# Kernel optimization log

Measured on AMD Instinct MI355X. Metric: run time of the kernel, lower is better.

Reference implementation:

```python
import jax, jax.numpy as jnp
import numpy as np

E = 384      # EMBEDDING_SIZE
DFF = 1536
H = 6        # NUM_HEADS
D = E // H   # ATTN_DIM_SIZE = 64
T = 256      # SEQ_LEN
L = 6        # NUM_BLOCKS
V = 65       # VOCAB_SIZE
NPOS = 10000.0
B = 128


def _pos_encoding():
    i = jnp.arange(T, dtype=jnp.float32)[:, None]
    k = jnp.arange(E // 2, dtype=jnp.float32)[None, :]
    ang = i / jnp.power(NPOS, 2.0 * k / E)   # [T, E/2]
    pe = jnp.zeros((T, E), dtype=jnp.float32)
    pe = pe.at[:, 0::2].set(jnp.sin(ang))
    pe = pe.at[:, 1::2].set(jnp.cos(ang))
    return pe


def setup_inputs() -> dict:
    key = jax.random.key(0)
    ks = jax.random.split(key, 24)
    s = 0.02
    n = lambda k, shp: (jax.random.normal(k, shp, dtype=jnp.float32) * s)
    inp = {
        'tokens': jax.random.randint(ks[0], (B, T), 0, V),
        'pos_enc': _pos_encoding(),
        'emb': n(ks[1], (V, E)),
        # stacked per-layer params [L, ...]; weights stored as (in, out)
        'Wq': n(ks[2], (L, E, E)), 'bq': jnp.zeros((L, E)),
        'Wk': n(ks[3], (L, E, E)), 'bk': jnp.zeros((L, E)),
        'Wv': n(ks[4], (L, E, E)), 'bv': jnp.zeros((L, E)),
        'Wo': n(ks[5], (L, E, E)), 'bo': jnp.zeros((L, E)),
        'ln1_g': jnp.ones((L, E)), 'ln1_b': jnp.zeros((L, E)),
        'W1': n(ks[6], (L, E, DFF)), 'c1': jnp.zeros((L, DFF)),
        'W2': n(ks[7], (L, DFF, E)), 'c2': jnp.zeros((L, E)),
        'ln2_g': jnp.ones((L, E)), 'ln2_b': jnp.zeros((L, E)),
        'Wl': n(ks[8], (E, V)), 'bl': jnp.zeros((V,)),
    }
    return inp


def _layer_norm(x, g, b, eps=1e-5):
    mu = jnp.mean(x, axis=-1, keepdims=True)
    var = jnp.mean((x - mu) ** 2, axis=-1, keepdims=True)
    return (x - mu) * jax.lax.rsqrt(var + eps) * g + b


def _decoder(tokens, pos_enc, emb, Wq, bq, Wk, bk, Wv, bv, Wo, bo,
             ln1_g, ln1_b, W1, c1, W2, c2, ln2_g, ln2_b, Wl, bl):
    b_, t_ = tokens.shape
    x = emb[tokens] + pos_enc[None, :t_, :]            # [B,T,E]
    causal = jnp.tril(jnp.ones((t_, t_), dtype=bool)) # tril mask
    scale = D ** (-0.5)

    def block(x, p):
        (wq, bq_, wk, bk_, wv, bv_, wo, bo_, g1, be1, w1, c1_, w2, c2_, g2, be2) = p
        h = _layer_norm(x, g1, be1)
        q = (h @ wq + bq_).reshape(b_, t_, H, D)
        k = (h @ wk + bk_).reshape(b_, t_, H, D)
        v = (h @ wv + bv_).reshape(b_, t_, H, D)
        scores = jnp.einsum('bqhd,bkhd->bhqk', q, k) * scale
        scores = jnp.where(causal[None, None], scores, -jnp.inf)
        attn = jax.nn.softmax(scores, axis=-1)
        o = jnp.einsum('bhqk,bkhd->bqhd', attn, v).reshape(b_, t_, E)
        x = x + (o @ wo + bo_)
        h2 = _layer_norm(x, g2, be2)
        x = x + (jax.nn.relu(h2 @ w1 + c1_) @ w2 + c2_)
        return x, None

    params = (Wq, bq, Wk, bk, Wv, bv, Wo, bo, ln1_g, ln1_b, W1, c1, W2, c2, ln2_g, ln2_b)
    x, _ = jax.lax.scan(block, x, params)
    return x @ Wl + bl                                 # [B,T,V]


def reference(tokens, pos_enc, emb, Wq, bq, Wk, bk, Wv, bv, Wo, bo,
              ln1_g, ln1_b, W1, c1, W2, c2, ln2_g, ln2_b, Wl, bl):
    return _decoder(tokens, pos_enc, emb, Wq, bq, Wk, bk, Wv, bv, Wo, bo,
                    ln1_g, ln1_b, W1, c1, W2, c2, ln2_g, ln2_b, Wl, bl)
```

## Files before the change

kernel.cpp:

```cpp
#include <hip/hip_runtime.h>
#include <hip/hip_bf16.h>
#include <stdint.h>

constexpr int E   = 384;
constexpr int DFF = 1536;
constexpr int NH  = 6;
constexpr int HD  = 64;
constexpr int T   = 256;
constexpr int NL  = 6;
constexpr int NV  = 65;
constexpr int BB  = 128;
constexpr int MTOT = BB * T;
constexpr int CB  = 32;

typedef __bf16 bf16;
typedef __attribute__((ext_vector_type(8))) __bf16 bf16x8;
typedef __attribute__((ext_vector_type(4))) __bf16 bf16x4;
typedef __attribute__((ext_vector_type(4))) float floatx4;

__device__ __forceinline__ void gload_lds16(const void* g, void* l) {
    __builtin_amdgcn_global_load_lds(
        (const __attribute__((address_space(1))) void*)g,
        (__attribute__((address_space(3))) void*)l, 16, 0, 0);
}

#define GBN 128

template <int MODE, int SWAP, int W>
__device__ __forceinline__ void gemm_body(
    char* AsB,
    const bf16* __restrict__ A, int lda,
    const bf16* __restrict__ Bf,
    const float* __restrict__ bias,
    void* __restrict__ Cv, void* __restrict__ Cv2, int ldc,
    int nt, int mt, int Nvalid, int K, int relu)
{
    constexpr int BM     = W * 32;
    constexpr int ABYTES = BM * 64;
    constexpr int SBUF   = ABYTES + 8192;

    int tid = threadIdx.x;
    int lane = tid & 63;
    int wid = tid >> 6;
    int wr = wid >> 1, wc = wid & 1;
    int lq = lane >> 4, lr = lane & 15;

    const bf16* Ab = A + (long)mt * BM * lda;

    int rp0 = wid * 8 + (lane >> 3);
    int s   = lane & 7;
    int sp  = s ^ (rp0 & 7);
    int rowA = 2 * rp0 + (sp >> 2);
    int kOff = (sp & 3) * 8;
    const bf16* srcA0 = Ab + (long)rowA * lda + kOff;
    const bf16* srcA1 = srcA0 + (long)(BM / 2) * lda;
    int dst0 = wid * 1024;
    int dst1 = W * 1024 + wid * 1024;

    int nks = K / 32;

    const bf16* srcB0;
    const bf16* srcB1 = nullptr;
    int dstB0, dstB1 = 0;
    if constexpr (W == 8) {
        srcB0 = Bf + ((long)(nt * 8 + wid) * nks) * 512 + lane * 8;
        dstB0 = ABYTES + wid * 1024;
    } else {
        srcB0 = Bf + ((long)(nt * 8 + wid * 2) * nks) * 512 + lane * 8;
        srcB1 = Bf + ((long)(nt * 8 + wid * 2 + 1) * nks) * 512 + lane * 8;
        dstB0 = ABYTES + (wid * 2) * 1024;
        dstB1 = ABYTES + (wid * 2 + 1) * 1024;
    }

    floatx4 acc[4][4];
#pragma unroll
    for (int i = 0; i < 4; i++)
#pragma unroll
        for (int j = 0; j < 4; j++) acc[i][j] = floatx4{0.f, 0.f, 0.f, 0.f};

    int afo = (wr * 32 + (lr >> 1)) * 128 +
              (((((lr & 1) << 2) | lq) ^ (lr >> 1)) << 4);
    int bfo = ABYTES + wc * 4096 + lane * 16;

    auto stage = [&](int ks, int bo) {
        long ka = (long)ks * 32;
        gload_lds16(srcA0 + ka, AsB + bo + dst0);
        gload_lds16(srcA1 + ka, AsB + bo + dst1);
        long kb = (long)ks * 512;
        gload_lds16(srcB0 + kb, AsB + bo + dstB0);
        if constexpr (W == 4)
            gload_lds16(srcB1 + kb, AsB + bo + dstB1);
    };

    int o0 = 0, o1 = SBUF, o2 = 2 * SBUF;

    stage(0, o0);
    if (nks > 1) {
        stage(1, o1);
        if constexpr (W == 8)
            asm volatile("s_waitcnt vmcnt(3)" ::: "memory");
        else
            asm volatile("s_waitcnt vmcnt(4)" ::: "memory");
    } else {
        asm volatile("s_waitcnt vmcnt(0)" ::: "memory");
    }
    __builtin_amdgcn_s_barrier();

    for (int ki = 0; ki < nks; ++ki) {
        if (ki + 2 < nks) stage(ki + 2, o2);
        __builtin_amdgcn_sched_barrier(0);

        bf16x8 bfr[4];
#pragma unroll
        for (int ni = 0; ni < 4; ni++)
            bfr[ni] = *(const bf16x8*)(AsB + o0 + bfo + ni * 1024);
        bf16x8 af[4];
#pragma unroll
        for (int mi = 0; mi < 4; mi++)
            af[mi] = *(const bf16x8*)(AsB + o0 + afo + mi * 1024);

        __builtin_amdgcn_s_setprio(1);
#pragma unroll
        for (int mi = 0; mi < 4; mi++)
#pragma unroll
            for (int ni = 0; ni < 4; ni++)
                acc[mi][ni] = SWAP
                    ? __builtin_amdgcn_mfma_f32_16x16x32_bf16(bfr[ni], af[mi], acc[mi][ni], 0, 0, 0)
                    : __builtin_amdgcn_mfma_f32_16x16x32_bf16(af[mi], bfr[ni], acc[mi][ni], 0, 0, 0);
        __builtin_amdgcn_s_setprio(0);

        if (ki + 1 < nks) {
            if (ki + 2 < nks) {
                if constexpr (W == 8)
                    asm volatile("s_waitcnt vmcnt(3) lgkmcnt(0)" ::: "memory");
                else
                    asm volatile("s_waitcnt vmcnt(4) lgkmcnt(0)" ::: "memory");
            } else {
                asm volatile("s_waitcnt vmcnt(0) lgkmcnt(0)" ::: "memory");
            }
            __builtin_amdgcn_s_barrier();
        }
        int t = o0; o0 = o1; o1 = o2; o2 = t;
    }

    int m0 = mt * BM, n0 = nt * GBN;
#pragma unroll
    for (int mi = 0; mi < 4; mi++) {
#pragma unroll
        for (int ni = 0; ni < 4; ni++) {
            floatx4 v = acc[mi][ni];
            if (SWAP) {
                int rowL = m0 + wr * 64 + mi * 16 + lr;
                int col0 = n0 + wc * 64 + ni * 16 + lq * 4;
                if (MODE == 5) {
                    bf16x4 pv;
#pragma unroll
                    for (int r = 0; r < 4; r++) pv[r] = (bf16)(v[r] + bias[col0 + r]);
                    *(bf16x4*)((bf16*)Cv + (long)rowL * 768 + col0) = pv;
                } else if (MODE == 1) {
                    bf16* Cp = (bf16*)Cv;
                    bf16x4* ptr = (bf16x4*)(Cp + (long)rowL * ldc + col0);
                    bf16x4 old = *ptr;
                    bf16x4 pv;
#pragma unroll
                    for (int r = 0; r < 4; r++)
                        pv[r] = (bf16)((float)old[r] + v[r] + bias[col0 + r]);
                    *ptr = pv;
                } else if (MODE == 4) {
                    float* Cp = (float*)Cv;
#pragma unroll
                    for (int r = 0; r < 4; r++)
                        if (col0 + r < Nvalid)
                            Cp[(long)rowL * ldc + col0 + r] = v[r] + bias[col0 + r];
                } else {
                    if (col0 < Nvalid) {
                        bf16x4 pv;
#pragma unroll
                        for (int r = 0; r < 4; r++) {
                            float x = v[r] + (bias ? bias[col0 + r] : 0.f);
                            if (relu) x = fmaxf(x, 0.f);
                            pv[r] = (bf16)x;
                        }
                        *(bf16x4*)((bf16*)Cv + (long)rowL * ldc + col0) = pv;
                    }
                }
            } else {
                int row0 = m0 + wr * 64 + mi * 16 + lq * 4;
                int colL = n0 + wc * 64 + ni * 16 + lr;
                float bv = bias[colL];
                bf16x4 pv;
#pragma unroll
                for (int r = 0; r < 4; r++) pv[r] = (bf16)(v[r] + bv);
                int bidx = row0 >> 8, pos = row0 & 255, e = colL - 768;
                *(bf16x4*)((bf16*)Cv2 + (long)bidx * (E * T) + (long)e * T + pos) = pv;
            }
        }
    }
}

template <int MODE, int W>
__global__ __launch_bounds__(W * 64, 4) void k_gemm(
    const bf16* __restrict__ A, int lda,
    const bf16* __restrict__ Bf,
    const float* __restrict__ bias,
    void* __restrict__ Cv, void* __restrict__ Cv2, int ldc,
    int Mtiles, int Ntiles, int Nvalid, int K,
    int relu)
{
    __shared__ __align__(16) char AsB[3 * (W * 32 * 64 + 8192)];

    int nb = gridDim.x;
    int per = nb >> 3;
    int bphys = blockIdx.x;
    int bid = (bphys & 7) * per + (bphys >> 3);

    int nt = bid % Ntiles;
    int mt = bid / Ntiles;

    if (MODE == 5 && nt >= 6)
        gemm_body<5, 0, W>(AsB, A, lda, Bf, bias, Cv, Cv2, ldc, nt, mt, Nvalid, K, relu);
    else
        gemm_body<MODE, 1, W>(AsB, A, lda, Bf, bias, Cv, Cv2, ldc, nt, mt, Nvalid, K, relu);
}

__global__ __launch_bounds__(256) void k_attn(
    const bf16* __restrict__ qk, const bf16* __restrict__ vt,
    bf16* __restrict__ o)
{
    int nb = gridDim.x;
    int per = nb >> 3;
    int bphys = blockIdx.x;
    int bid = (bphys & 7) * per + (bphys >> 3);

    int qt = bid & 3; bid >>= 2;
    int h = bid % NH; int b = bid / NH;
    int tid = threadIdx.x;
    int lane = tid & 63;
    int w = tid >> 6;
    int lq = lane >> 4;
    int lr = lane & 15;

    __shared__ __align__(16) bf16 Ks[256 * 72];
    __shared__ __align__(16) bf16 Vs[64 * 264];

    const bf16* qbase = qk + (long)(b * T + qt * 64 + w * 16) * 768 + h * 64;
    const bf16* kbase = qk + (long)(b * T) * 768 + 384 + h * 64;
    const bf16* vbase = vt + ((long)b * E + h * 64) * T;

#pragma unroll
    for (int i = 0; i < 8; i++) {
        int idx = i * 256 + tid;
        int row = idx >> 3, off = (idx & 7) * 8;
        *(bf16x8*)(&Ks[row * 72 + off]) = *(const bf16x8*)(kbase + (long)row * 768 + off);
    }
#pragma unroll
    for (int i = 0; i < 8; i++) {
        int idx = i * 256 + tid;
        int row = idx >> 5, off = (idx & 31) * 8;
        *(bf16x8*)(&Vs[row * 264 + off]) = *(const bf16x8*)(vbase + (long)row * 256 + off);
    }

    bf16x8 aq0 = *(const bf16x8*)(qbase + (long)lr * 768 + lq * 8);
    bf16x8 aq1 = *(const bf16x8*)(qbase + (long)lr * 768 + 32 + lq * 8);

    __syncthreads();

    const int ntmax = qt * 4 + 3;
    floatx4 zero = {0.f, 0.f, 0.f, 0.f};
    floatx4 s[16];
#pragma unroll
    for (int nt = 0; nt < 16; nt++) s[nt] = zero;

#pragma unroll
    for (int nt = 0; nt < 16; nt++) {
        if (nt <= ntmax) {
            const bf16* kp = &Ks[(nt * 16 + lr) * 72 + lq * 8];
            bf16x8 b0 = *(const bf16x8*)(kp);
            bf16x8 b1 = *(const bf16x8*)(kp + 32);
            s[nt] = __builtin_amdgcn_mfma_f32_16x16x32_bf16(aq0, b0, s[nt], 0, 0, 0);
            s[nt] = __builtin_amdgcn_mfma_f32_16x16x32_bf16(aq1, b1, s[nt], 0, 0, 0);
        }
    }

    int trow0 = qt * 64 + w * 16 + lq * 4;
    float m4[4] = {-3e38f, -3e38f, -3e38f, -3e38f};
#pragma unroll
    for (int nt = 0; nt < 16; nt++) {
        if (nt <= ntmax) {
            int tc = nt * 16 + lr;
#pragma unroll
            for (int r = 0; r < 4; r++) {
                float v = s[nt][r] * 0.125f;
                if (tc > trow0 + r) v = -3e38f;
                s[nt][r] = v;
                m4[r] = fmaxf(m4[r], v);
            }
        }
    }
#pragma unroll
    for (int r = 0; r < 4; r++) {
#pragma unroll
        for (int off = 1; off < 16; off <<= 1)
            m4[r] = fmaxf(m4[r], __shfl_xor(m4[r], off, 64));
    }

    float l4[4] = {0.f, 0.f, 0.f, 0.f};
#pragma unroll
    for (int nt = 0; nt < 16; nt++) {
        if (nt <= ntmax) {
#pragma unroll
            for (int r = 0; r < 4; r++) {
                float pv = __expf(s[nt][r] - m4[r]);
                l4[r] += pv;
                s[nt][r] = pv;
            }
        }
    }
#pragma unroll
    for (int r = 0; r < 4; r++) {
#pragma unroll
        for (int off = 1; off < 16; off <<= 1)
            l4[r] += __shfl_xor(l4[r], off, 64);
    }

    __syncthreads();

    bf16* P = Ks + w * (16 * 264);
#pragma unroll
    for (int nt = 0; nt < 16; nt++) {
        if (nt <= ntmax) {
#pragma unroll
            for (int r = 0; r < 4; r++)
                P[(lq * 4 + r) * 264 + nt * 16 + lr] = (bf16)s[nt][r];
        }
    }

    floatx4 oacc[4];
#pragma unroll
    for (int nd = 0; nd < 4; nd++) oacc[nd] = zero;
    const int kkmax = 2 * (qt + 1);
#pragma unroll
    for (int kk = 0; kk < 8; kk++) {
        if (kk < kkmax) {
            bf16x8 ap = *(const bf16x8*)(&P[lr * 264 + kk * 32 + lq * 8]);
#pragma unroll
            for (int nd = 0; nd < 4; nd++) {
                bf16x8 bv = *(const bf16x8*)(&Vs[(nd * 16 + lr) * 264 + kk * 32 + lq * 8]);
                oacc[nd] = __builtin_amdgcn_mfma_f32_16x16x32_bf16(ap, bv, oacc[nd], 0, 0, 0);
            }
        }
    }

#pragma unroll
    for (int r = 0; r < 4; r++) {
        float inv = 1.0f / l4[r];
        long rowg = (long)b * T + trow0 + r;
#pragma unroll
        for (int nd = 0; nd < 4; nd++) {
            o[rowg * E + h * 64 + nd * 16 + lr] = (bf16)(oacc[nd][r] * inv);
        }
    }
}

__global__ void k_ln(const bf16* __restrict__ x, const float* __restrict__ g,
                     const float* __restrict__ b, bf16* __restrict__ h) {
    int row = blockIdx.x * 4 + (threadIdx.x >> 6);
    int lane = threadIdx.x & 63;
    const bf16* xr = x + (long)row * E;
    float v[6];
    float s = 0.f;
#pragma unroll
    for (int i = 0; i < 6; i++) { v[i] = (float)xr[lane + 64 * i]; s += v[i]; }
#pragma unroll
    for (int o = 1; o < 64; o <<= 1) s += __shfl_xor(s, o, 64);
    float mu = s * (1.0f / E);
    float q = 0.f;
#pragma unroll
    for (int i = 0; i < 6; i++) { float d = v[i] - mu; q += d * d; }
#pragma unroll
    for (int o = 1; o < 64; o <<= 1) q += __shfl_xor(q, o, 64);
    float rs = rsqrtf(q * (1.0f / E) + 1e-5f);
    bf16* hr = h + (long)row * E;
#pragma unroll
    for (int i = 0; i < 6; i++) {
        int c = lane + 64 * i;
        hr[c] = (bf16)((v[i] - mu) * rs * g[c] + b[c]);
    }
}

__global__ void k_transpose_frag(const float* __restrict__ W, bf16* __restrict__ Wf,
                                 int K, int N, int NPAD) {
    long idx = (long)blockIdx.x * 256 + threadIdx.x;
    long per = (long)NPAD * K;
    int l = (int)(idx / per);
    long r = idx - (long)l * per;
    int j = (int)(r & 7); r >>= 3;
    int lane = (int)(r & 63); r >>= 6;
    int nks = K / 32;
    int ks = (int)(r % nks);
    int c16 = (int)(r / nks);
    int col = c16 * 16 + (lane & 15);
    int k = ks * 32 + (lane >> 4) * 8 + j;
    Wf[idx] = (col < N) ? (bf16)W[((long)l * K + k) * N + col] : (bf16)0.0f;
}

__global__ void k_transpose_qkv_frag(const float* __restrict__ Wq, const float* __restrict__ Wk,
                                     const float* __restrict__ Wv, bf16* __restrict__ Wf) {
    long idx = (long)blockIdx.x * 256 + threadIdx.x;
    long per = (long)1152 * E;
    int l = (int)(idx / per);
    long r = idx - (long)l * per;
    int j = (int)(r & 7); r >>= 3;
    int lane = (int)(r & 63); r >>= 6;
    int nks = E / 32;
    int ks = (int)(r % nks);
    int c16 = (int)(r / nks);
    int col = c16 * 16 + (lane & 15);
    int k = ks * 32 + (lane >> 4) * 8 + j;
    const float* src;
    int cc;
    if (col < 384)      { src = Wq; cc = col; }
    else if (col < 768) { src = Wk; cc = col - 384; }
    else                { src = Wv; cc = col - 768; }
    Wf[idx] = (bf16)src[((long)l * E + k) * E + cc];
}

__global__ void k_bias_qkv(const float* __restrict__ bq, const float* __restrict__ bk,
                           const float* __restrict__ bv, float* __restrict__ bqkv) {
    int idx = blockIdx.x * 256 + threadIdx.x;
    int l = idx / 1152;
    int j = idx - l * 1152;
    const float* src;
    int jj;
    if (j < 384)      { src = bq; jj = j; }
    else if (j < 768) { src = bk; jj = j - 384; }
    else              { src = bv; jj = j - 768; }
    bqkv[idx] = src[l * E + jj];
}

__global__ void k_embed(const int* __restrict__ tokens, const float* __restrict__ pos,
                        const float* __restrict__ emb, bf16* __restrict__ x) {
    long idx = (long)blockIdx.x * 256 + threadIdx.x;
    int e = (int)(idx % E);
    long bt = idx / E;
    int t = (int)(bt % T);
    int tok = tokens[bt];
    x[idx] = (bf16)(emb[(long)tok * E + e] + pos[(long)t * E + e]);
}

extern "C" void kernel_launch(void* const* d_in, const int* in_sizes, int n_in,
                              void* d_out, int out_size, void* d_ws, size_t ws_size,
                              hipStream_t stream) {
    const int*   tokens = (const int*)d_in[0];
    const float* pos  = (const float*)d_in[1];
    const float* emb  = (const float*)d_in[2];
    const float* Wq   = (const float*)d_in[3];
    const float* bq   = (const float*)d_in[4];
    const float* Wk   = (const float*)d_in[5];
    const float* bk   = (const float*)d_in[6];
    const float* Wv   = (const float*)d_in[7];
    const float* bv   = (const float*)d_in[8];
    const float* Wo   = (const float*)d_in[9];
    const float* bo   = (const float*)d_in[10];
    const float* g1   = (const float*)d_in[11];
    const float* be1  = (const float*)d_in[12];
    const float* W1   = (const float*)d_in[13];
    const float* c1   = (const float*)d_in[14];
    const float* W2   = (const float*)d_in[15];
    const float* c2   = (const float*)d_in[16];
    const float* g2   = (const float*)d_in[17];
    const float* be2  = (const float*)d_in[18];
    const float* Wl   = (const float*)d_in[19];
    const float* bl   = (const float*)d_in[20];

    char* p = (char*)d_ws;
    bf16* x  = (bf16*)p;   p += (long)MTOT * E * 2;
    bf16* h  = (bf16*)p;   p += (long)MTOT * E * 2;
    bf16* qk = (bf16*)p;   p += (long)MTOT * 768 * 2;
    bf16* vt = (bf16*)p;   p += (long)BB * E * T * 2;
    bf16* SP = (bf16*)p;   p += (long)CB * NH * T * T * 2;
    bf16* WqkvF = (bf16*)p; p += (long)NL * 1152 * E * 2;
    bf16* WoF = (bf16*)p;  p += (long)NL * E * E * 2;
    bf16* W1F = (bf16*)p;  p += (long)NL * DFF * E * 2;
    bf16* W2F = (bf16*)p;  p += (long)NL * E * DFF * 2;
    bf16* WlF = (bf16*)p;  p += (long)128 * E * 2;
    float* bqkv = (float*)p; p += (long)NL * 1152 * 4;
    bf16* mid = qk;
    bf16* o   = h;
    (void)SP;

    k_transpose_qkv_frag<<<(NL * 1152 * E) / 256, 256, 0, stream>>>(Wq, Wk, Wv, WqkvF);
    k_transpose_frag<<<(NL * E * E) / 256, 256, 0, stream>>>(Wo, WoF, E, E, E);
    k_transpose_frag<<<(NL * DFF * E) / 256, 256, 0, stream>>>(W1, W1F, E, DFF, DFF);
    k_transpose_frag<<<(NL * E * DFF) / 256, 256, 0, stream>>>(W2, W2F, DFF, E, E);
    k_transpose_frag<<<(128 * E) / 256, 256, 0, stream>>>(Wl, WlF, E, NV, 128);
    k_bias_qkv<<<(NL * 1152) / 256, 256, 0, stream>>>(bq, bk, bv, bqkv);

    k_embed<<<(MTOT * E) / 256, 256, 0, stream>>>(tokens, pos, emb, x);

    for (int l = 0; l < NL; l++) {
        k_ln<<<MTOT / 4, 256, 0, stream>>>(x, g1 + l * E, be1 + l * E, h);
        k_gemm<5, 8><<<128 * 9, 512, 0, stream>>>(h, E, WqkvF + (long)l * 1152 * E,
                                                  bqkv + l * 1152, qk, vt, 0,
                                                  128, 9, 1152, E, 0);
        k_attn<<<BB * NH * 4, 256, 0, stream>>>(qk, vt, o);
        k_gemm<1, 4><<<256 * 3, 256, 0, stream>>>(o, E, WoF + (long)l * E * E,
                                                  bo + l * E, x, nullptr, E,
                                                  256, 3, E, E, 0);
        k_ln<<<MTOT / 4, 256, 0, stream>>>(x, g2 + l * E, be2 + l * E, h);
        k_gemm<0, 8><<<128 * 12, 512, 0, stream>>>(h, E, W1F + (long)l * DFF * E,
                                                   c1 + l * DFF, mid, nullptr, DFF,
                                                   128, 12, DFF, E, 1);
        k_gemm<1, 4><<<256 * 3, 256, 0, stream>>>(mid, DFF, W2F + (long)l * E * DFF,
                                                  c2 + l * E, x, nullptr, E,
                                                  256, 3, E, DFF, 0);
    }

    k_gemm<4, 4><<<256 * 1, 256, 0, stream>>>(x, E, WlF,
                                              bl, d_out, nullptr, NV,
                                              256, 1, NV, E, 0);
}
```

Before: 1.701 ms.

## Add 256x128 four-wave GEMM kernel with larger per-wave tiles for layer GEMMs

Adds a GEMM variant that runs 256 threads on a 256x128 output tile. Each wave owns 64 rows by all 128 columns, using a 4x8 grid of MFMA accumulators. This raises arithmetic intensity per LDS fragment load and halves the block count for the Wo and W2 GEMMs, which previously used 128-row tiles. All four per-layer GEMMs now use it, while the old kernel is pared down to the final logits projection. The cost is higher register pressure (128 accumulator floats per lane, launch bounds of 2 blocks per CU) and fewer blocks per launch, which can hurt occupancy and wave balance.

```diff
diff --git a/kernel.cpp b/kernel.cpp
--- a/kernel.cpp
+++ b/kernel.cpp
@@ -25,6 +25,179 @@
 }
 
 #define GBN 128
+
+template <int MODE, int SWAP>
+__device__ __forceinline__ void gemm2_body(
+    char* AsB,
+    const bf16* __restrict__ A, int lda,
+    const bf16* __restrict__ Bf,
+    const float* __restrict__ bias,
+    void* __restrict__ Cv, void* __restrict__ Cv2, int ldc,
+    int nt, int mt, int Nvalid, int K, int relu)
+{
+    constexpr int BM     = 256;
+    constexpr int ABYTES = 16384;
+    constexpr int SBUF   = ABYTES + 8192;
+
+    int tid = threadIdx.x;
+    int lane = tid & 63;
+    int wid = tid >> 6;
+    int lq = lane >> 4, lr = lane & 15;
+
+    const bf16* Ab = A + (long)mt * BM * lda;
+
+    int rpw = wid * 32 + (lane >> 3);
+    int sp  = (lane & 7) ^ ((lane >> 3) & 7);
+    int rowA = 2 * rpw + (sp >> 2);
+    int kOff = (sp & 3) * 8;
+    const bf16* srcA = Ab + (long)rowA * lda + kOff;
+    const long aG = 16 * (long)lda;
+    int dstA = wid * 4096;
+
+    int nks = K / 32;
+
+    const bf16* srcB0 = Bf + ((long)(nt * 8 + wid * 2) * nks) * 512 + lane * 8;
+    const bf16* srcB1 = srcB0 + (long)nks * 512;
+    int dstB0 = ABYTES + (wid * 2) * 1024;
+    int dstB1 = dstB0 + 1024;
+
+    floatx4 acc[4][8];
+#pragma unroll
+    for (int i = 0; i < 4; i++)
+#pragma unroll
+        for (int j = 0; j < 8; j++) acc[i][j] = floatx4{0.f, 0.f, 0.f, 0.f};
+
+    int afo = wid * 4096 + (lr >> 1) * 128 +
+              (((((lr & 1) << 2) | lq) ^ (lr >> 1)) << 4);
+    int bfo = ABYTES + lane * 16;
+
+    auto stage = [&](int ks, int bo) {
+        long ka = (long)ks * 32;
+#pragma unroll
+        for (int g = 0; g < 4; g++)
+            gload_lds16(srcA + g * aG + ka, AsB + bo + dstA + g * 1024);
+        long kb = (long)ks * 512;
+        gload_lds16(srcB0 + kb, AsB + bo + dstB0);
+        gload_lds16(srcB1 + kb, AsB + bo + dstB1);
+    };
+
+    int o0 = 0, o1 = SBUF, o2 = 2 * SBUF;
+
+    stage(0, o0);
+    if (nks > 1) {
+        stage(1, o1);
+        asm volatile("s_waitcnt vmcnt(6)" ::: "memory");
+    } else {
+        asm volatile("s_waitcnt vmcnt(0)" ::: "memory");
+    }
+    __builtin_amdgcn_s_barrier();
+
+    for (int ki = 0; ki < nks; ++ki) {
+        if (ki + 2 < nks) stage(ki + 2, o2);
+        __builtin_amdgcn_sched_barrier(0);
+
+        bf16x8 af[4];
+#pragma unroll
+        for (int mi = 0; mi < 4; mi++)
+            af[mi] = *(const bf16x8*)(AsB + o0 + afo + mi * 1024);
+        bf16x8 bfr[8];
+#pragma unroll
+        for (int ni = 0; ni < 8; ni++)
+            bfr[ni] = *(const bf16x8*)(AsB + o0 + bfo + ni * 1024);
+
+        __builtin_amdgcn_s_setprio(1);
+#pragma unroll
+        for (int mi = 0; mi < 4; mi++)
+#pragma unroll
+            for (int ni = 0; ni < 8; ni++)
+                acc[mi][ni] = SWAP
+                    ? __builtin_amdgcn_mfma_f32_16x16x32_bf16(bfr[ni], af[mi], acc[mi][ni], 0, 0, 0)
+                    : __builtin_amdgcn_mfma_f32_16x16x32_bf16(af[mi], bfr[ni], acc[mi][ni], 0, 0, 0);
+        __builtin_amdgcn_s_setprio(0);
+
+        if (ki + 1 < nks) {
+            if (ki + 2 < nks)
+                asm volatile("s_waitcnt vmcnt(6) lgkmcnt(0)" ::: "memory");
+            else
+                asm volatile("s_waitcnt vmcnt(0) lgkmcnt(0)" ::: "memory");
+            __builtin_amdgcn_s_barrier();
+        }
+        int t = o0; o0 = o1; o1 = o2; o2 = t;
+    }
+
+    int m0 = mt * BM, n0 = nt * GBN;
+#pragma unroll
+    for (int mi = 0; mi < 4; mi++) {
+#pragma unroll
+        for (int ni = 0; ni < 8; ni++) {
+            floatx4 v = acc[mi][ni];
+            if (SWAP) {
+                int rowL = m0 + wid * 64 + mi * 16 + lr;
+                int col0 = n0 + ni * 16 + lq * 4;
+                if (MODE == 5) {
+                    bf16x4 pv;
+#pragma unroll
+                    for (int r = 0; r < 4; r++) pv[r] = (bf16)(v[r] + bias[col0 + r]);
+                    *(bf16x4*)((bf16*)Cv + (long)rowL * 768 + col0) = pv;
+                } else if (MODE == 1) {
+                    bf16* Cp = (bf16*)Cv;
+                    bf16x4* ptr = (bf16x4*)(Cp + (long)rowL * ldc + col0);
+                    bf16x4 old = *ptr;
+                    bf16x4 pv;
+#pragma unroll
+                    for (int r = 0; r < 4; r++)
+                        pv[r] = (bf16)((float)old[r] + v[r] + bias[col0 + r]);
+                    *ptr = pv;
+                } else {
+                    if (col0 < Nvalid) {
+                        bf16x4 pv;
+#pragma unroll
+                        for (int r = 0; r < 4; r++) {
+                            float x = v[r] + (bias ? bias[col0 + r] : 0.f);
+                            if (relu) x = fmaxf(x, 0.f);
+                            pv[r] = (bf16)x;
+                        }
+                        *(bf16x4*)((bf16*)Cv + (long)rowL * ldc + col0) = pv;
+                    }
+                }
+            } else {
+                int row0 = m0 + wid * 64 + mi * 16 + lq * 4;
+                int colL = n0 + ni * 16 + lr;
+                float bv = bias[colL];
+                bf16x4 pv;
+#pragma unroll
+                for (int r = 0; r < 4; r++) pv[r] = (bf16)(v[r] + bv);
+                int bidx = row0 >> 8, pos = row0 & 255, e = colL - 768;
+                *(bf16x4*)((bf16*)Cv2 + (long)bidx * (E * T) + (long)e * T + pos) = pv;
+            }
+        }
+    }
+}
+
+template <int MODE>
+__global__ __launch_bounds__(256, 2) void k_gemm2(
+    const bf16* __restrict__ A, int lda,
+    const bf16* __restrict__ Bf,
+    const float* __restrict__ bias,
+    void* __restrict__ Cv, void* __restrict__ Cv2, int ldc,
+    int Mtiles, int Ntiles, int Nvalid, int K,
+    int relu)
+{
+    __shared__ __align__(16) char AsB[3 * 24576];
+
+    int nb = gridDim.x;
+    int per = nb >> 3;
+    int bphys = blockIdx.x;
+    int bid = (bphys & 7) * per + (bphys >> 3);
+
+    int nt = bid % Ntiles;
+    int mt = bid / Ntiles;
+
+    if (MODE == 5 && nt >= 6)
+        gemm2_body<5, 0>(AsB, A, lda, Bf, bias, Cv, Cv2, ldc, nt, mt, Nvalid, K, relu);
+    else
+        gemm2_body<MODE, 1>(AsB, A, lda, Bf, bias, Cv, Cv2, ldc, nt, mt, Nvalid, K, relu);
+}
 
 template <int MODE, int SWAP, int W>
 __device__ __forceinline__ void gemm_body(
@@ -59,18 +232,10 @@
 
     int nks = K / 32;
 
-    const bf16* srcB0;
-    const bf16* srcB1 = nullptr;
-    int dstB0, dstB1 = 0;
-    if constexpr (W == 8) {
-        srcB0 = Bf + ((long)(nt * 8 + wid) * nks) * 512 + lane * 8;
-        dstB0 = ABYTES + wid * 1024;
-    } else {
-        srcB0 = Bf + ((long)(nt * 8 + wid * 2) * nks) * 512 + lane * 8;
-        srcB1 = Bf + ((long)(nt * 8 + wid * 2 + 1) * nks) * 512 + lane * 8;
-        dstB0 = ABYTES + (wid * 2) * 1024;
-        dstB1 = ABYTES + (wid * 2 + 1) * 1024;
-    }
+    const bf16* srcB0 = Bf + ((long)(nt * 8 + wid * 2) * nks) * 512 + lane * 8;
+    const bf16* srcB1 = Bf + ((long)(nt * 8 + wid * 2 + 1) * nks) * 512 + lane * 8;
+    int dstB0 = ABYTES + (wid * 2) * 1024;
+    int dstB1 = ABYTES + (wid * 2 + 1) * 1024;
 
     floatx4 acc[4][4];
 #pragma unroll
@@ -88,8 +253,7 @@
         gload_lds16(srcA1 + ka, AsB + bo + dst1);
         long kb = (long)ks * 512;
         gload_lds16(srcB0 + kb, AsB + bo + dstB0);
-        if constexpr (W == 4)
-            gload_lds16(srcB1 + kb, AsB + bo + dstB1);
+        gload_lds16(srcB1 + kb, AsB + bo + dstB1);
     };
 
     int o0 = 0, o1 = SBUF, o2 = 2 * SBUF;
@@ -97,10 +261,7 @@
     stage(0, o0);
     if (nks > 1) {
         stage(1, o1);
-        if constexpr (W == 8)
-            asm volatile("s_waitcnt vmcnt(3)" ::: "memory");
-        else
-            asm volatile("s_waitcnt vmcnt(4)" ::: "memory");
+        asm volatile("s_waitcnt vmcnt(4)" ::: "memory");
     } else {
         asm volatile("s_waitcnt vmcnt(0)" ::: "memory");
     }
@@ -130,14 +291,10 @@
         __builtin_amdgcn_s_setprio(0);
 
         if (ki + 1 < nks) {
-            if (ki + 2 < nks) {
-                if constexpr (W == 8)
-                    asm volatile("s_waitcnt vmcnt(3) lgkmcnt(0)" ::: "memory");
-                else
-                    asm volatile("s_waitcnt vmcnt(4) lgkmcnt(0)" ::: "memory");
-            } else {
+            if (ki + 2 < nks)
+                asm volatile("s_waitcnt vmcnt(4) lgkmcnt(0)" ::: "memory");
+            else
                 asm volatile("s_waitcnt vmcnt(0) lgkmcnt(0)" ::: "memory");
-            }
             __builtin_amdgcn_s_barrier();
         }
         int t = o0; o0 = o1; o1 = o2; o2 = t;
@@ -149,50 +306,25 @@
 #pragma unroll
         for (int ni = 0; ni < 4; ni++) {
             floatx4 v = acc[mi][ni];
-            if (SWAP) {
-                int rowL = m0 + wr * 64 + mi * 16 + lr;
-                int col0 = n0 + wc * 64 + ni * 16 + lq * 4;
-                if (MODE == 5) {
+            int rowL = m0 + wr * 64 + mi * 16 + lr;
+            int col0 = n0 + wc * 64 + ni * 16 + lq * 4;
+            if (MODE == 4) {
+                float* Cp = (float*)Cv;
+#pragma unroll
+                for (int r = 0; r < 4; r++)
+                    if (col0 + r < Nvalid)
+                        Cp[(long)rowL * ldc + col0 + r] = v[r] + bias[col0 + r];
+            } else {
+                if (col0 < Nvalid) {
                     bf16x4 pv;
 #pragma unroll
-                    for (int r = 0; r < 4; r++) pv[r] = (bf16)(v[r] + bias[col0 + r]);
-                    *(bf16x4*)((bf16*)Cv + (long)rowL * 768 + col0) = pv;
-                } else if (MODE == 1) {
-                    bf16* Cp = (bf16*)Cv;
-                    bf16x4* ptr = (bf16x4*)(Cp + (long)rowL * ldc + col0);
-                    bf16x4 old = *ptr;
-                    bf16x4 pv;
-#pragma unroll
-                    for (int r = 0; r < 4; r++)
-                        pv[r] = (bf16)((float)old[r] + v[r] + bias[col0 + r]);
-                    *ptr = pv;
-                } else if (MODE == 4) {
-                    float* Cp = (float*)Cv;
-#pragma unroll
-                    for (int r = 0; r < 4; r++)
-                        if (col0 + r < Nvalid)
-                            Cp[(long)rowL * ldc + col0 + r] = v[r] + bias[col0 + r];
-                } else {
-                    if (col0 < Nvalid) {
-                        bf16x4 pv;
-#pragma unroll
-                        for (int r = 0; r < 4; r++) {
-                            float x = v[r] + (bias ? bias[col0 + r] : 0.f);
-                            if (relu) x = fmaxf(x, 0.f);
-                            pv[r] = (bf16)x;
-                        }
-                        *(bf16x4*)((bf16*)Cv + (long)rowL * ldc + col0) = pv;
+                    for (int r = 0; r < 4; r++) {
+                        float x = v[r] + (bias ? bias[col0 + r] : 0.f);
+                        if (relu) x = fmaxf(x, 0.f);
+                        pv[r] = (bf16)x;
                     }
+                    *(bf16x4*)((bf16*)Cv + (long)rowL * ldc + col0) = pv;
                 }
-            } else {
-                int row0 = m0 + wr * 64 + mi * 16 + lq * 4;
-                int colL = n0 + wc * 64 + ni * 16 + lr;
-                float bv = bias[colL];
-                bf16x4 pv;
-#pragma unroll
-                for (int r = 0; r < 4; r++) pv[r] = (bf16)(v[r] + bv);
-                int bidx = row0 >> 8, pos = row0 & 255, e = colL - 768;
-                *(bf16x4*)((bf16*)Cv2 + (long)bidx * (E * T) + (long)e * T + pos) = pv;
             }
         }
     }
@@ -217,10 +349,7 @@
     int nt = bid % Ntiles;
     int mt = bid / Ntiles;
 
-    if (MODE == 5 && nt >= 6)
-        gemm_body<5, 0, W>(AsB, A, lda, Bf, bias, Cv, Cv2, ldc, nt, mt, Nvalid, K, relu);
-    else
-        gemm_body<MODE, 1, W>(AsB, A, lda, Bf, bias, Cv, Cv2, ldc, nt, mt, Nvalid, K, relu);
+    gemm_body<MODE, 1, W>(AsB, A, lda, Bf, bias, Cv, Cv2, ldc, nt, mt, Nvalid, K, relu);
 }
 
 __global__ __launch_bounds__(256) void k_attn(
@@ -500,20 +629,20 @@
 
     for (int l = 0; l < NL; l++) {
         k_ln<<<MTOT / 4, 256, 0, stream>>>(x, g1 + l * E, be1 + l * E, h);
-        k_gemm<5, 8><<<128 * 9, 512, 0, stream>>>(h, E, WqkvF + (long)l * 1152 * E,
-                                                  bqkv + l * 1152, qk, vt, 0,
-                                                  128, 9, 1152, E, 0);
+        k_gemm2<5><<<128 * 9, 256, 0, stream>>>(h, E, WqkvF + (long)l * 1152 * E,
+                                                bqkv + l * 1152, qk, vt, 0,
+                                                128, 9, 1152, E, 0);
         k_attn<<<BB * NH * 4, 256, 0, stream>>>(qk, vt, o);
-        k_gemm<1, 4><<<256 * 3, 256, 0, stream>>>(o, E, WoF + (long)l * E * E,
-                                                  bo + l * E, x, nullptr, E,
-                                                  256, 3, E, E, 0);
+        k_gemm2<1><<<128 * 3, 256, 0, stream>>>(o, E, WoF + (long)l * E * E,
+                                                bo + l * E, x, nullptr, E,
+                                                128, 3, E, E, 0);
         k_ln<<<MTOT / 4, 256, 0, stream>>>(x, g2 + l * E, be2 + l * E, h);
-        k_gemm<0, 8><<<128 * 12, 512, 0, stream>>>(h, E, W1F + (long)l * DFF * E,
-                                                   c1 + l * DFF, mid, nullptr, DFF,
-                                                   128, 12, DFF, E, 1);
-        k_gemm<1, 4><<<256 * 3, 256, 0, stream>>>(mid, DFF, W2F + (long)l * E * DFF,
-                                                  c2 + l * E, x, nullptr, E,
-                                                  256, 3, E, DFF, 0);
+        k_gemm2<0><<<128 * 12, 256, 0, stream>>>(h, E, W1F + (long)l * DFF * E,
+                                                 c1 + l * DFF, mid, nullptr, DFF,
+                                                 128, 12, DFF, E, 1);
+        k_gemm2<1><<<128 * 3, 256, 0, stream>>>(mid, DFF, W2F + (long)l * E * DFF,
+                                                c2 + l * E, x, nullptr, E,
+                                                128, 3, E, DFF, 0);
     }
 
     k_gemm<4, 4><<<256 * 1, 256, 0, stream>>>(x, E, WlF,
```

After: 1.859 ms. 9.3% more time.

## Add 256x256-tile GEMM kernel with 8-phase double-buffered schedule for layer GEMMs

Applied to the files above, without the earlier changes.

Introduces a new GEMM kernel using 256x256 output tiles with 8 waves, each computing 128x64, and a K-step of 64 staged through two 64KB LDS buffers. The loop is split into interleaved load/MFMA phases separated by barriers. Column tiles that do not divide evenly are shifted back and their overlapping outputs masked. The QKV, Wo, W1 and W2 GEMMs switch to it, which raises data reuse per block and reduces the block count. The costs are higher register and LDS pressure, fewer blocks to fill the CUs, and redundant compute on overlapping edge tiles.

```diff
diff --git a/kernel.cpp b/kernel.cpp
--- a/kernel.cpp
+++ b/kernel.cpp
@@ -24,15 +24,233 @@
         (__attribute__((address_space(3))) void*)l, 16, 0, 0);
 }
 
-#define GBN 128
-
-template <int MODE, int SWAP, int W>
+#define SBUF8 65536
+
+template <int MODE, int SWAP>
+__device__ __forceinline__ void gemm8_body(
+    char* L,
+    const bf16* __restrict__ A, int lda,
+    const bf16* __restrict__ Bf,
+    const float* __restrict__ bias,
+    void* __restrict__ Cv, void* __restrict__ Cv2, int ldc,
+    int n0, int sLo, int mt, int Ncols, int K, int relu)
+{
+    int tid = threadIdx.x;
+    int lane = tid & 63;
+    int wid = tid >> 6;
+    int wm = wid >> 2;
+    int wn = wid & 3;
+    int lq = lane >> 4, lr = lane & 15;
+
+    const bf16* Ab = A + (long)mt * 256 * lda;
+    int nks = K / 32;
+    int NT  = K / 64;
+
+    int l3 = lane >> 3;
+    int sp = (lane & 7) ^ l3;
+    int kO = (sp & 3) * 8;
+    int rowA0 = (wid * 2 + 0) * 16 + 2 * l3 + (sp >> 2);
+    int rowA1 = (wid * 2 + 1) * 16 + 2 * l3 + (sp >> 2);
+    const bf16* srcA0 = Ab + (long)rowA0 * lda + kO;
+    const bf16* srcA1 = Ab + (long)rowA1 * lda + kO;
+    int dstA0 = (wid * 2 + 0) * 1024;
+    int dstA1 = (wid * 2 + 1) * 1024;
+
+    int c16b = n0 >> 4;
+    const bf16* srcB0 = Bf + ((long)(c16b + wid * 2 + 0) * nks) * 512 + lane * 8;
+    const bf16* srcB1 = Bf + ((long)(c16b + wid * 2 + 1) * nks) * 512 + lane * 8;
+    int dstB0 = 32768 + (wid * 2 + 0) * 2048;
+    int dstB1 = 32768 + (wid * 2 + 1) * 2048;
+
+    int aro = wm * 8192 + (lr >> 1) * 128 +
+              (((((lr & 1) << 2) | lq) ^ ((lr >> 1) & 7)) << 4);
+    int bro = 32768 + (wn * 4) * 2048 + lane * 16;
+
+    floatx4 acc[8][4];
+#pragma unroll
+    for (int i = 0; i < 8; i++)
+#pragma unroll
+        for (int j = 0; j < 4; j++) acc[i][j] = floatx4{0.f, 0.f, 0.f, 0.f};
+
+    bf16x8 af[4][2];
+    bf16x8 bq[2][2][2];
+
+#define STAGE_A8(KT, BO) { long ko_ = (long)(KT) * 64;                          \
+    gload_lds16(srcA0 + ko_,      L + (BO) + dstA0);                            \
+    gload_lds16(srcA0 + ko_ + 32, L + (BO) + 16384 + dstA0);                    \
+    gload_lds16(srcA1 + ko_,      L + (BO) + dstA1);                            \
+    gload_lds16(srcA1 + ko_ + 32, L + (BO) + 16384 + dstA1); }
+
+#define STAGE_B8(KT, BO) {                                                      \
+    gload_lds16(srcB0 + ((long)(KT) * 2    ) * 512, L + (BO) + dstB0);          \
+    gload_lds16(srcB0 + ((long)(KT) * 2 + 1) * 512, L + (BO) + dstB0 + 1024);   \
+    gload_lds16(srcB1 + ((long)(KT) * 2    ) * 512, L + (BO) + dstB1);          \
+    gload_lds16(srcB1 + ((long)(KT) * 2 + 1) * 512, L + (BO) + dstB1 + 1024); }
+
+#define LOAD_A8(MQ, BO) { _Pragma("unroll")                                     \
+    for (int s_ = 0; s_ < 2; s_++) { _Pragma("unroll")                          \
+      for (int m4_ = 0; m4_ < 4; m4_++)                                         \
+        af[m4_][s_] = *(const bf16x8*)(L + (BO) + s_ * 16384 +                  \
+                                       ((MQ) * 4 + m4_) * 1024 + aro); } }
+
+#define LOAD_B8(NQ, BO) { _Pragma("unroll")                                     \
+    for (int s_ = 0; s_ < 2; s_++) { _Pragma("unroll")                          \
+      for (int n2_ = 0; n2_ < 2; n2_++)                                         \
+        bq[NQ][n2_][s_] = *(const bf16x8*)(L + (BO) + bro +                     \
+                                           ((NQ) * 2 + n2_) * 2048 + s_ * 1024); } }
+
+#define QMFMA8(MQ, NQ) { _Pragma("unroll")                                      \
+    for (int s_ = 0; s_ < 2; s_++) { _Pragma("unroll")                          \
+      for (int m4_ = 0; m4_ < 4; m4_++) { _Pragma("unroll")                     \
+        for (int n2_ = 0; n2_ < 2; n2_++) {                                     \
+          if (SWAP)                                                             \
+            acc[(MQ)*4+m4_][(NQ)*2+n2_] = __builtin_amdgcn_mfma_f32_16x16x32_bf16( \
+                bq[NQ][n2_][s_], af[m4_][s_], acc[(MQ)*4+m4_][(NQ)*2+n2_], 0,0,0); \
+          else                                                                  \
+            acc[(MQ)*4+m4_][(NQ)*2+n2_] = __builtin_amdgcn_mfma_f32_16x16x32_bf16( \
+                af[m4_][s_], bq[NQ][n2_][s_], acc[(MQ)*4+m4_][(NQ)*2+n2_], 0,0,0); } } } }
+
+#define PH_SYNC { __builtin_amdgcn_s_barrier();                                 \
+    asm volatile("s_waitcnt lgkmcnt(0)" ::: "memory");                          \
+    __builtin_amdgcn_sched_barrier(0); }
+#define VM0_ asm volatile("s_waitcnt vmcnt(0)" ::: "memory")
+
+    STAGE_A8(0, 0); STAGE_B8(0, 0);
+    VM0_;
+    __builtin_amdgcn_s_barrier();
+
+    int nit = NT >> 1;
+    for (int it = 0; it < nit; ++it) {
+        int t = it * 2;
+        LOAD_A8(0, 0); LOAD_B8(0, 0);
+        STAGE_A8(t + 1, SBUF8);
+        PH_SYNC;
+        __builtin_amdgcn_s_setprio(1); QMFMA8(0, 0); __builtin_amdgcn_s_setprio(0);
+        __builtin_amdgcn_s_barrier();
+        LOAD_B8(1, 0);
+        STAGE_B8(t + 1, SBUF8);
+        PH_SYNC;
+        __builtin_amdgcn_s_setprio(1); QMFMA8(0, 1); __builtin_amdgcn_s_setprio(0);
+        __builtin_amdgcn_s_barrier();
+        LOAD_A8(1, 0);
+        PH_SYNC;
+        __builtin_amdgcn_s_setprio(1); QMFMA8(1, 0); __builtin_amdgcn_s_setprio(0);
+        __builtin_amdgcn_s_barrier();
+        __builtin_amdgcn_s_setprio(1); QMFMA8(1, 1); __builtin_amdgcn_s_setprio(0);
+        VM0_;
+        __builtin_amdgcn_s_barrier();
+        LOAD_A8(0, SBUF8); LOAD_B8(0, SBUF8);
+        if (t + 2 < NT) STAGE_A8(t + 2, 0);
+        PH_SYNC;
+        __builtin_amdgcn_s_setprio(1); QMFMA8(0, 0); __builtin_amdgcn_s_setprio(0);
+        __builtin_amdgcn_s_barrier();
+        LOAD_B8(1, SBUF8);
+        if (t + 2 < NT) STAGE_B8(t + 2, 0);
+        PH_SYNC;
+        __builtin_amdgcn_s_setprio(1); QMFMA8(0, 1); __builtin_amdgcn_s_setprio(0);
+        __builtin_amdgcn_s_barrier();
+        LOAD_A8(1, SBUF8);
+        PH_SYNC;
+        __builtin_amdgcn_s_setprio(1); QMFMA8(1, 0); __builtin_amdgcn_s_setprio(0);
+        __builtin_amdgcn_s_barrier();
+        __builtin_amdgcn_s_setprio(1); QMFMA8(1, 1); __builtin_amdgcn_s_setprio(0);
+        VM0_;
+        __builtin_amdgcn_s_barrier();
+    }
+
+    int m0 = mt * 256;
+#pragma unroll
+    for (int mi = 0; mi < 8; mi++) {
+#pragma unroll
+        for (int nf = 0; nf < 4; nf++) {
+            floatx4 v = acc[mi][nf];
+            if (SWAP) {
+                int rowL = m0 + wm * 128 + mi * 16 + lr;
+                int col0 = n0 + wn * 64 + nf * 16 + lq * 4;
+                if (col0 >= sLo) {
+                    if (MODE == 5) {
+                        bf16x4 pv;
+#pragma unroll
+                        for (int r = 0; r < 4; r++) pv[r] = (bf16)(v[r] + bias[col0 + r]);
+                        *(bf16x4*)((bf16*)Cv + (long)rowL * 768 + col0) = pv;
+                    } else if (MODE == 1) {
+                        bf16* Cp = (bf16*)Cv;
+                        bf16x4* ptr = (bf16x4*)(Cp + (long)rowL * ldc + col0);
+                        bf16x4 old = *ptr;
+                        bf16x4 pv;
+#pragma unroll
+                        for (int r = 0; r < 4; r++)
+                            pv[r] = (bf16)((float)old[r] + v[r] + bias[col0 + r]);
+                        *ptr = pv;
+                    } else {
+                        bf16x4 pv;
+#pragma unroll
+                        for (int r = 0; r < 4; r++) {
+                            float x = v[r] + (bias ? bias[col0 + r] : 0.f);
+                            if (relu) x = fmaxf(x, 0.f);
+                            pv[r] = (bf16)x;
+                        }
+                        *(bf16x4*)((bf16*)Cv + (long)rowL * ldc + col0) = pv;
+                    }
+                }
+            } else {
+                int row0 = m0 + wm * 128 + mi * 16 + lq * 4;
+                int colL = n0 + wn * 64 + nf * 16 + lr;
+                if (colL >= sLo) {
+                    float bv = bias[colL];
+                    bf16x4 pv;
+#pragma unroll
+                    for (int r = 0; r < 4; r++) pv[r] = (bf16)(v[r] + bv);
+                    int bidx = row0 >> 8, pos = row0 & 255, e = colL - 768;
+                    *(bf16x4*)((bf16*)Cv2 + (long)bidx * (E * T) + (long)e * T + pos) = pv;
+                }
+            }
+        }
+    }
+#undef STAGE_A8
+#undef STAGE_B8
+#undef LOAD_A8
+#undef LOAD_B8
+#undef QMFMA8
+#undef PH_SYNC
+#undef VM0_
+}
+
+template <int MODE>
+__global__ __launch_bounds__(512, 2) void k_gemm8(
+    const bf16* __restrict__ A, int lda,
+    const bf16* __restrict__ Bf,
+    const float* __restrict__ bias,
+    void* __restrict__ Cv, void* __restrict__ Cv2, int ldc,
+    int Mtiles, int Ntiles, int Ncols, int K,
+    int relu)
+{
+    __shared__ __align__(16) char L[2 * SBUF8];
+
+    int nb = gridDim.x;
+    int per = nb >> 3;
+    int bphys = blockIdx.x;
+    int bid = (bphys & 7) * per + (bphys >> 3);
+
+    int nt = bid % Ntiles;
+    int mt = bid / Ntiles;
+
+    int n0 = nt * 256, sLo = 0;
+    if (n0 + 256 > Ncols) { sLo = n0; n0 = Ncols - 256; }
+
+    if (MODE == 5 && n0 >= 768)
+        gemm8_body<5, 0>(L, A, lda, Bf, bias, Cv, Cv2, ldc, n0, sLo, mt, Ncols, K, relu);
+    else
+        gemm8_body<MODE, 1>(L, A, lda, Bf, bias, Cv, Cv2, ldc, n0, sLo, mt, Ncols, K, relu);
+}
+
+template <int MODE, int W>
 __device__ __forceinline__ void gemm_body(
     char* AsB,
     const bf16* __restrict__ A, int lda,
     const bf16* __restrict__ Bf,
     const float* __restrict__ bias,
-    void* __restrict__ Cv, void* __restrict__ Cv2, int ldc,
+    void* __restrict__ Cv, int ldc,
     int nt, int mt, int Nvalid, int K, int relu)
 {
     constexpr int BM     = W * 32;
@@ -59,18 +277,10 @@
 
     int nks = K / 32;
 
-    const bf16* srcB0;
-    const bf16* srcB1 = nullptr;
-    int dstB0, dstB1 = 0;
-    if constexpr (W == 8) {
-        srcB0 = Bf + ((long)(nt * 8 + wid) * nks) * 512 + lane * 8;
-        dstB0 = ABYTES + wid * 1024;
-    } else {
-        srcB0 = Bf + ((long)(nt * 8 + wid * 2) * nks) * 512 + lane * 8;
-        srcB1 = Bf + ((long)(nt * 8 + wid * 2 + 1) * nks) * 512 + lane * 8;
-        dstB0 = ABYTES + (wid * 2) * 1024;
-        dstB1 = ABYTES + (wid * 2 + 1) * 1024;
-    }
+    const bf16* srcB0 = Bf + ((long)(nt * 8 + wid * 2) * nks) * 512 + lane * 8;
+    const bf16* srcB1 = Bf + ((long)(nt * 8 + wid * 2 + 1) * nks) * 512 + lane * 8;
+    int dstB0 = ABYTES + (wid * 2) * 1024;
+    int dstB1 = ABYTES + (wid * 2 + 1) * 1024;
 
     floatx4 acc[4][4];
 #pragma unroll
@@ -88,8 +298,7 @@
         gload_lds16(srcA1 + ka, AsB + bo + dst1);
         long kb = (long)ks * 512;
         gload_lds16(srcB0 + kb, AsB + bo + dstB0);
-        if constexpr (W == 4)
-            gload_lds16(srcB1 + kb, AsB + bo + dstB1);
+        gload_lds16(srcB1 + kb, AsB + bo + dstB1);
     };
 
     int o0 = 0, o1 = SBUF, o2 = 2 * SBUF;
@@ -97,10 +306,7 @@
     stage(0, o0);
     if (nks > 1) {
         stage(1, o1);
-        if constexpr (W == 8)
-            asm volatile("s_waitcnt vmcnt(3)" ::: "memory");
-        else
-            asm volatile("s_waitcnt vmcnt(4)" ::: "memory");
+        asm volatile("s_waitcnt vmcnt(4)" ::: "memory");
     } else {
         asm volatile("s_waitcnt vmcnt(0)" ::: "memory");
     }
@@ -124,75 +330,34 @@
         for (int mi = 0; mi < 4; mi++)
 #pragma unroll
             for (int ni = 0; ni < 4; ni++)
-                acc[mi][ni] = SWAP
-                    ? __builtin_amdgcn_mfma_f32_16x16x32_bf16(bfr[ni], af[mi], acc[mi][ni], 0, 0, 0)
-                    : __builtin_amdgcn_mfma_f32_16x16x32_bf16(af[mi], bfr[ni], acc[mi][ni], 0, 0, 0);
+                acc[mi][ni] = __builtin_amdgcn_mfma_f32_16x16x32_bf16(
+                    bfr[ni], af[mi], acc[mi][ni], 0, 0, 0);
         __builtin_amdgcn_s_setprio(0);
 
         if (ki + 1 < nks) {
-            if (ki + 2 < nks) {
-                if constexpr (W == 8)
-                    asm volatile("s_waitcnt vmcnt(3) lgkmcnt(0)" ::: "memory");
-                else
-                    asm volatile("s_waitcnt vmcnt(4) lgkmcnt(0)" ::: "memory");
-            } else {
+            if (ki + 2 < nks)
+                asm volatile("s_waitcnt vmcnt(4) lgkmcnt(0)" ::: "memory");
+            else
                 asm volatile("s_waitcnt vmcnt(0) lgkmcnt(0)" ::: "memory");
-            }
             __builtin_amdgcn_s_barrier();
         }
         int t = o0; o0 = o1; o1 = o2; o2 = t;
     }
 
-    int m0 = mt * BM, n0 = nt * GBN;
+    int m0 = mt * BM, n0 = nt * 128;
 #pragma unroll
     for (int mi = 0; mi < 4; mi++) {
 #pragma unroll
         for (int ni = 0; ni < 4; ni++) {
             floatx4 v = acc[mi][ni];
-            if (SWAP) {
-                int rowL = m0 + wr * 64 + mi * 16 + lr;
-                int col0 = n0 + wc * 64 + ni * 16 + lq * 4;
-                if (MODE == 5) {
-                    bf16x4 pv;
-#pragma unroll
-                    for (int r = 0; r < 4; r++) pv[r] = (bf16)(v[r] + bias[col0 + r]);
-                    *(bf16x4*)((bf16*)Cv + (long)rowL * 768 + col0) = pv;
-                } else if (MODE == 1) {
-                    bf16* Cp = (bf16*)Cv;
-                    bf16x4* ptr = (bf16x4*)(Cp + (long)rowL * ldc + col0);
-                    bf16x4 old = *ptr;
-                    bf16x4 pv;
-#pragma unroll
-                    for (int r = 0; r < 4; r++)
-                        pv[r] = (bf16)((float)old[r] + v[r] + bias[col0 + r]);
-                    *ptr = pv;
-                } else if (MODE == 4) {
-                    float* Cp = (float*)Cv;
-#pragma unroll
-                    for (int r = 0; r < 4; r++)
-                        if (col0 + r < Nvalid)
-                            Cp[(long)rowL * ldc + col0 + r] = v[r] + bias[col0 + r];
-                } else {
-                    if (col0 < Nvalid) {
-                        bf16x4 pv;
-#pragma unroll
-                        for (int r = 0; r < 4; r++) {
-                            float x = v[r] + (bias ? bias[col0 + r] : 0.f);
-                            if (relu) x = fmaxf(x, 0.f);
-                            pv[r] = (bf16)x;
-                        }
-                        *(bf16x4*)((bf16*)Cv + (long)rowL * ldc + col0) = pv;
-                    }
-                }
-            } else {
-                int row0 = m0 + wr * 64 + mi * 16 + lq * 4;
-                int colL = n0 + wc * 64 + ni * 16 + lr;
-                float bv = bias[colL];
-                bf16x4 pv;
-#pragma unroll
-                for (int r = 0; r < 4; r++) pv[r] = (bf16)(v[r] + bv);
-                int bidx = row0 >> 8, pos = row0 & 255, e = colL - 768;
-                *(bf16x4*)((bf16*)Cv2 + (long)bidx * (E * T) + (long)e * T + pos) = pv;
+            int rowL = m0 + wr * 64 + mi * 16 + lr;
+            int col0 = n0 + wc * 64 + ni * 16 + lq * 4;
+            if (MODE == 4) {
+                float* Cp = (float*)Cv;
+#pragma unroll
+                for (int r = 0; r < 4; r++)
+                    if (col0 + r < Nvalid)
+                        Cp[(long)rowL * ldc + col0 + r] = v[r] + bias[col0 + r];
             }
         }
     }
@@ -217,10 +382,7 @@
     int nt = bid % Ntiles;
     int mt = bid / Ntiles;
 
-    if (MODE == 5 && nt >= 6)
-        gemm_body<5, 0, W>(AsB, A, lda, Bf, bias, Cv, Cv2, ldc, nt, mt, Nvalid, K, relu);
-    else
-        gemm_body<MODE, 1, W>(AsB, A, lda, Bf, bias, Cv, Cv2, ldc, nt, mt, Nvalid, K, relu);
+    gemm_body<MODE, W>(AsB, A, lda, Bf, bias, Cv, ldc, nt, mt, Nvalid, K, relu);
 }
 
 __global__ __launch_bounds__(256) void k_attn(
@@ -500,20 +662,20 @@
 
     for (int l = 0; l < NL; l++) {
         k_ln<<<MTOT / 4, 256, 0, stream>>>(x, g1 + l * E, be1 + l * E, h);
-        k_gemm<5, 8><<<128 * 9, 512, 0, stream>>>(h, E, WqkvF + (long)l * 1152 * E,
-                                                  bqkv + l * 1152, qk, vt, 0,
-                                                  128, 9, 1152, E, 0);
+        k_gemm8<5><<<128 * 5, 512, 0, stream>>>(h, E, WqkvF + (long)l * 1152 * E,
+                                                bqkv + l * 1152, qk, vt, 0,
+                                                128, 5, 1152, E, 0);
         k_attn<<<BB * NH * 4, 256, 0, stream>>>(qk, vt, o);
-        k_gemm<1, 4><<<256 * 3, 256, 0, stream>>>(o, E, WoF + (long)l * E * E,
-                                                  bo + l * E, x, nullptr, E,
-                                                  256, 3, E, E, 0);
+        k_gemm8<1><<<128 * 2, 512, 0, stream>>>(o, E, WoF + (long)l * E * E,
+                                                bo + l * E, x, nullptr, E,
+                                                128, 2, 384, E, 0);
         k_ln<<<MTOT / 4, 256, 0, stream>>>(x, g2 + l * E, be2 + l * E, h);
-        k_gemm<0, 8><<<128 * 12, 512, 0, stream>>>(h, E, W1F + (long)l * DFF * E,
-                                                   c1 + l * DFF, mid, nullptr, DFF,
-                                                   128, 12, DFF, E, 1);
-        k_gemm<1, 4><<<256 * 3, 256, 0, stream>>>(mid, DFF, W2F + (long)l * E * DFF,
-                                                  c2 + l * E, x, nullptr, E,
-                                                  256, 3, E, DFF, 0);
+        k_gemm8<0><<<128 * 6, 512, 0, stream>>>(h, E, W1F + (long)l * DFF * E,
+                                                c1 + l * DFF, mid, nullptr, DFF,
+                                                128, 6, 1536, E, 1);
+        k_gemm8<1><<<128 * 2, 512, 0, stream>>>(mid, DFF, W2F + (long)l * E * DFF,
+                                                c2 + l * E, x, nullptr, E,
+                                                128, 2, 384, DFF, 0);
     }
 
     k_gemm<4, 4><<<256 * 1, 256, 0, stream>>>(x, E, WlF,
```

Result: slower. 1.964 ms (+15.5%).
